# Kernel tuning notes

Measured on AMD Instinct MI355X. Metric: run time of the kernel, lower is better.

The kernel has to match this reference:

```python
import jax, jax.numpy as jnp
import numpy as np

N = 20000        # nodes
E = 160000       # directed edges (self-loops added in reference, as PyG GATConv does)
IN = 128         # in_channels
OUT = 128        # out_channels
H = 36           # heads of conv1 (head kwarg)
C = 36           # per-head channels of conv1 (== head kwarg)
HID = H * C      # 1296, conv1 concat output
NEG_SLOPE = 0.2  # PyG GATConv default


def gat_layer(x, src, dst, W, a_src, a_dst, bias, heads, ch, concat, num_nodes):
    """One PyG-style GATConv (eval mode, self-loops already in src/dst)."""
    h = (x @ W).reshape(num_nodes, heads, ch)               # [N,H,C]
    alpha_s = jnp.sum(h * a_src, axis=-1)                   # [N,H]
    alpha_d = jnp.sum(h * a_dst, axis=-1)                   # [N,H]
    e = jax.nn.leaky_relu(alpha_s[src] + alpha_d[dst], NEG_SLOPE)  # [E,H]
    # segment softmax over incoming edges of each target node
    m = jax.ops.segment_max(e, dst, num_segments=num_nodes)        # [N,H]
    m = jnp.where(jnp.isfinite(m), m, 0.0)                  # nodes with no in-edges
    ex = jnp.exp(e - m[dst])                                # [E,H]
    denom = jax.ops.segment_sum(ex, dst, num_segments=num_nodes)   # [N,H]
    alpha = ex / (denom[dst] + 1e-16)                       # [E,H]
    # weighted scatter-aggregate of source features
    out = jax.ops.segment_sum(h[src] * alpha[:, :, None], dst, num_segments=num_nodes)  # [N,H,C]
    out = out.reshape(num_nodes, heads * ch) if concat else out.mean(axis=1)
    return out + bias


def setup_inputs() -> dict:
    key = jax.random.key(0)
    ks = jax.random.split(key, 12)
    x = jax.random.normal(ks[0], (N, IN), jnp.float32)
    edge_index = jax.random.randint(ks[1], (2, E), 0, N, dtype=jnp.int64)
    # conv1 params: heads=36, out per head=36, concat
    W1 = jax.random.normal(ks[2], (IN, H * C), jnp.float32) / np.float32(np.sqrt(IN))
    a_src1 = jax.random.normal(ks[3], (H, C), jnp.float32) * 0.1
    a_dst1 = jax.random.normal(ks[4], (H, C), jnp.float32) * 0.1
    b1 = jnp.zeros((HID,), jnp.float32)
    # conv2 params: heads=1, out=OUT, no concat
    W2 = jax.random.normal(ks[5], (HID, OUT), jnp.float32) / np.float32(np.sqrt(HID))
    a_src2 = jax.random.normal(ks[6], (1, OUT), jnp.float32) * 0.1
    a_dst2 = jax.random.normal(ks[7], (1, OUT), jnp.float32) * 0.1
    b2 = jnp.zeros((OUT,), jnp.float32)
    return {"x": x, "edge_index": edge_index,
            "W1": W1, "a_src1": a_src1, "a_dst1": a_dst1, "b1": b1,
            "W2": W2, "a_src2": a_src2, "a_dst2": a_dst2, "b2": b2}


def reference(x, edge_index, W1, a_src1, a_dst1, b1, W2, a_src2, a_dst2, b2):
    num_nodes = x.shape[0]
    loop = jnp.arange(num_nodes, dtype=edge_index.dtype)
    src = jnp.concatenate([edge_index[0], loop])   # add self-loops (PyG default)
    dst = jnp.concatenate([edge_index[1], loop])
    h = jax.nn.relu(gat_layer(x, src, dst, W1, a_src1, a_dst1, b1,
                              heads=H, ch=C, concat=True, num_nodes=num_nodes))
    out = jax.nn.relu(gat_layer(h, src, dst, W2, a_src2, a_dst2, b2,
                                heads=1, ch=OUT, concat=False, num_nodes=num_nodes))
    return out
```

## Files before the change

kernel.cpp:

```cpp
#include <hip/hip_runtime.h>

#define N_NODES 20000
#define E_EDGES 160000
#define ET (E_EDGES + N_NODES)
#define IN_CH 128
#define HID 1296
#define HEADS 36
#define CPH 36
#define OUT_CH 128
#define KP2 1344
#define NEG_SLOPE 0.2f

typedef __attribute__((ext_vector_type(8))) short bf16x8;
typedef __attribute__((ext_vector_type(4))) float floatx4;

__device__ __forceinline__ float bf2f(unsigned short u) {
    union { unsigned int i; float f; } c; c.i = ((unsigned int)u) << 16; return c.f;
}
__device__ __forceinline__ unsigned short f2bf(float f) {
    union { float f; unsigned int i; } c; c.f = f;
    unsigned int r = c.i + 0x7FFF + ((c.i >> 16) & 1);
    return (unsigned short)(r >> 16);
}

__global__ __launch_bounds__(256) void k_castx(const float* __restrict__ x,
                                               unsigned short* __restrict__ xb) {
    int i = blockIdx.x * 256 + threadIdx.x;
    if (i >= N_NODES * IN_CH / 4) return;
    float4 v = ((const float4*)x)[i];
    ushort4 o; o.x = f2bf(v.x); o.y = f2bf(v.y); o.z = f2bf(v.z); o.w = f2bf(v.w);
    ((ushort4*)xb)[i] = o;
}

__global__ __launch_bounds__(256) void k_w1t(const float* __restrict__ W1,
                                             unsigned short* __restrict__ W1T) {
    int gid = blockIdx.x * 256 + threadIdx.x;
    if (gid >= HID * IN_CH) return;
    int n = gid >> 7, k = gid & 127;
    W1T[gid] = f2bf(W1[(size_t)k * HID + n]);
}

__global__ __launch_bounds__(256) void k_w2t(const float* __restrict__ W2,
                                             unsigned short* __restrict__ W2T) {
    int gid = blockIdx.x * 256 + threadIdx.x;
    if (gid >= OUT_CH * KP2) return;
    int n = gid / KP2, k = gid - n * KP2;
    W2T[gid] = (k < HID) ? f2bf(W2[(size_t)k * OUT_CH + n]) : 0;
}

__global__ __launch_bounds__(256) void k_gemm1(const unsigned short* __restrict__ xb,
                                               const unsigned short* __restrict__ W1T,
                                               unsigned short* __restrict__ h1b) {
    __shared__ unsigned short As[128][136];
    __shared__ unsigned short Bs[64][136];
    int tid = threadIdx.x;
    int r0 = blockIdx.x * 128;
    int n0 = blockIdx.y * 64;
#pragma unroll
    for (int i = 0; i < 8; i++) {
        int c = tid + i * 256;
        int row = c >> 4, kc = (c & 15) * 8;
        int gr = min(r0 + row, N_NODES - 1);
        *(bf16x8*)&As[row][kc] = *(const bf16x8*)(xb + (size_t)gr * IN_CH + kc);
    }
#pragma unroll
    for (int i = 0; i < 4; i++) {
        int c = tid + i * 256;
        int row = c >> 4, kc = (c & 15) * 8;
        int gn = min(n0 + row, HID - 1);
        *(bf16x8*)&Bs[row][kc] = *(const bf16x8*)(W1T + (size_t)gn * IN_CH + kc);
    }
    __syncthreads();
    int lane = tid & 63, w = tid >> 6;
    int quad = lane >> 4, l15 = lane & 15;
    int mbase = w * 32;
    floatx4 acc[2][4];
#pragma unroll
    for (int i = 0; i < 2; i++)
#pragma unroll
        for (int j = 0; j < 4; j++) acc[i][j] = (floatx4){0.f, 0.f, 0.f, 0.f};
#pragma unroll
    for (int kc = 0; kc < 128; kc += 32) {
        bf16x8 a0 = *(const bf16x8*)&As[mbase + l15][kc + quad * 8];
        bf16x8 a1 = *(const bf16x8*)&As[mbase + 16 + l15][kc + quad * 8];
#pragma unroll
        for (int j = 0; j < 4; j++) {
            bf16x8 b = *(const bf16x8*)&Bs[j * 16 + l15][kc + quad * 8];
            acc[0][j] = __builtin_amdgcn_mfma_f32_16x16x32_bf16(a0, b, acc[0][j], 0, 0, 0);
            acc[1][j] = __builtin_amdgcn_mfma_f32_16x16x32_bf16(a1, b, acc[1][j], 0, 0, 0);
        }
    }
#pragma unroll
    for (int i = 0; i < 2; i++)
#pragma unroll
        for (int j = 0; j < 4; j++) {
            int colc = n0 + j * 16 + l15;
            if (colc >= HID) continue;
#pragma unroll
            for (int r = 0; r < 4; r++) {
                int row = r0 + mbase + i * 16 + quad * 4 + r;
                if (row < N_NODES)
                    h1b[(size_t)row * HID + colc] = f2bf(acc[i][j][r]);
            }
        }
}

__global__ __launch_bounds__(256) void k_gemm2(const unsigned short* __restrict__ A,
                                               const unsigned short* __restrict__ W2T,
                                               float* __restrict__ h2a,
                                               float* __restrict__ h2b) {
    __shared__ unsigned short As[64][40];
    __shared__ unsigned short Bs[128][40];
    int tid = threadIdx.x;
    int r0 = blockIdx.x * 64;
    int kbase = blockIdx.y * 672;
    int lane = tid & 63, w = tid >> 6;
    int quad = lane >> 4, l15 = lane & 15;
    int mbase = (w & 1) * 32;
    int nbase = (w >> 1) * 64;
    floatx4 acc[2][4];
#pragma unroll
    for (int i = 0; i < 2; i++)
#pragma unroll
        for (int j = 0; j < 4; j++) acc[i][j] = (floatx4){0.f, 0.f, 0.f, 0.f};

    for (int it = 0; it < 21; it++) {
        int k0 = kbase + it * 32;
        __syncthreads();
        {
            int row = tid >> 2, kc = (tid & 3) * 8;
            int gr = min(r0 + row, N_NODES - 1);
            *(bf16x8*)&As[row][kc] = *(const bf16x8*)(A + (size_t)gr * KP2 + k0 + kc);
        }
        {
#pragma unroll
            for (int i = 0; i < 2; i++) {
                int c = tid + i * 256;
                int row = c >> 2, kc = (c & 3) * 8;
                *(bf16x8*)&Bs[row][kc] = *(const bf16x8*)(W2T + (size_t)row * KP2 + k0 + kc);
            }
        }
        __syncthreads();
        bf16x8 a0 = *(const bf16x8*)&As[mbase + l15][quad * 8];
        bf16x8 a1 = *(const bf16x8*)&As[mbase + 16 + l15][quad * 8];
#pragma unroll
        for (int j = 0; j < 4; j++) {
            bf16x8 b = *(const bf16x8*)&Bs[nbase + j * 16 + l15][quad * 8];
            acc[0][j] = __builtin_amdgcn_mfma_f32_16x16x32_bf16(a0, b, acc[0][j], 0, 0, 0);
            acc[1][j] = __builtin_amdgcn_mfma_f32_16x16x32_bf16(a1, b, acc[1][j], 0, 0, 0);
        }
    }
    float* dst = (blockIdx.y == 0) ? h2a : h2b;
#pragma unroll
    for (int i = 0; i < 2; i++)
#pragma unroll
        for (int j = 0; j < 4; j++) {
            int colc = nbase + j * 16 + l15;
#pragma unroll
            for (int r = 0; r < 4; r++) {
                int row = r0 + mbase + i * 16 + quad * 4 + r;
                if (row < N_NODES)
                    dst[(size_t)row * OUT_CH + colc] = acc[i][j][r];
            }
        }
}

__global__ __launch_bounds__(256) void k_alpha1(const unsigned short* __restrict__ h1b,
                                                const float* __restrict__ a_src,
                                                const float* __restrict__ a_dst,
                                                float* __restrict__ as,
                                                float* __restrict__ ad) {
    __shared__ float s_a[HEADS * CPH], s_b[HEADS * CPH];
    int tid = threadIdx.x;
    for (int i = tid; i < HEADS * CPH; i += 256) { s_a[i] = a_src[i]; s_b[i] = a_dst[i]; }
    __syncthreads();
    int gid = blockIdx.x * 256 + tid;
    if (gid >= N_NODES * HEADS) return;
    int n = gid / HEADS, h = gid - n * HEADS;
    const unsigned short* row = h1b + (size_t)n * HID + h * CPH;
    float ss = 0.f, sd = 0.f;
#pragma unroll
    for (int c = 0; c < CPH; c += 2) {
        uint u = *(const uint*)(row + c);
        float v0 = bf2f((unsigned short)(u & 0xFFFF));
        float v1 = bf2f((unsigned short)(u >> 16));
        ss += v0 * s_a[h * CPH + c] + v1 * s_a[h * CPH + c + 1];
        sd += v0 * s_b[h * CPH + c] + v1 * s_b[h * CPH + c + 1];
    }
    as[gid] = ss;
    ad[gid] = sd;
}

__global__ void k_count(const int* __restrict__ ei, int* __restrict__ cnt) {
    int e = blockIdx.x * 256 + threadIdx.x;
    if (e >= ET) return;
    int d = (e < E_EDGES) ? ei[E_EDGES + e] : (e - E_EDGES);
    atomicAdd(&cnt[d], 1);
}

__global__ __launch_bounds__(1024) void k_scan(const int* __restrict__ cnt, int* __restrict__ rowp) {
    __shared__ int sh[1024];
    const int PER = 20;
    int t = threadIdx.x;
    int base = t * PER;
    int local[PER];
    int sum = 0;
    for (int i = 0; i < PER; i++) {
        int idx = base + i;
        int v = (idx < N_NODES) ? cnt[idx] : 0;
        local[i] = sum;
        sum += v;
    }
    sh[t] = sum;
    __syncthreads();
    for (int off = 1; off < 1024; off <<= 1) {
        int v = (t >= off) ? sh[t - off] : 0;
        __syncthreads();
        sh[t] += v;
        __syncthreads();
    }
    int offset = (t == 0) ? 0 : sh[t - 1];
    for (int i = 0; i < PER; i++) {
        int idx = base + i;
        if (idx < N_NODES) rowp[idx] = offset + local[i];
    }
    if (t == 1023) rowp[N_NODES] = sh[1023];
}

__global__ void k_fill(const int* __restrict__ ei, const int* __restrict__ rowp,
                       int* __restrict__ cursor, int* __restrict__ col,
                       int* __restrict__ dstn) {
    int e = blockIdx.x * 256 + threadIdx.x;
    if (e >= ET) return;
    int s, d;
    if (e < E_EDGES) { s = ei[e]; d = ei[E_EDGES + e]; }
    else { s = e - E_EDGES; d = s; }
    int pos = rowp[d] + atomicAdd(&cursor[d], 1);
    col[pos] = s;
    dstn[pos] = d;
}

__global__ __launch_bounds__(256) void k_w1(const float* __restrict__ as1,
                                            const float* __restrict__ ad1,
                                            const int* __restrict__ col,
                                            const int* __restrict__ dstn,
                                            float* __restrict__ w) {
    int gid = blockIdx.x * 256 + threadIdx.x;
    if (gid >= ET * HEADS) return;
    int p = gid / HEADS, h = gid - p * HEADS;
    int s = col[p], d = dstn[p];
    float v = as1[(size_t)s * HEADS + h] + ad1[(size_t)d * HEADS + h];
    v = (v > 0.f) ? v : NEG_SLOPE * v;
    w[gid] = __expf(v);
}

__global__ __launch_bounds__(256) void k_agg1(const unsigned short* __restrict__ h1b,
                                              const float* __restrict__ w,
                                              const int* __restrict__ rowp,
                                              const int* __restrict__ col,
                                              const float* __restrict__ b1,
                                              unsigned short* __restrict__ out1b) {
    int n = blockIdx.x;
    int tid = threadIdx.x;
    int r0 = rowp[n], r1 = rowp[n + 1];
    __shared__ float inv[HEADS];
    __shared__ float wsh[32 * HEADS];
    __shared__ int   csh[32];
    if (tid < HEADS) {
        float den = 0.f;
        for (int p = r0; p < r1; p++) den += w[(size_t)p * HEADS + tid];
        inv[tid] = 1.f / (den + 1e-16f);
    }
    __syncthreads();
    float4 acc0 = {0.f, 0.f, 0.f, 0.f}, acc1 = {0.f, 0.f, 0.f, 0.f};
    int s1 = tid;
    int s2 = tid + 256;
    int h1i = s1 / 9;
    int h2i = (s2 < 324) ? s2 / 9 : 0;
    for (int p0 = r0; p0 < r1; p0 += 32) {
        int ne = min(32, r1 - p0);
        __syncthreads();
        for (int i = tid; i < ne * HEADS; i += 256) {
            int h = i % HEADS;
            wsh[i] = w[(size_t)p0 * HEADS + i] * inv[h];
        }
        if (tid < ne) csh[tid] = col[p0 + tid];
        __syncthreads();
        for (int e = 0; e < ne; e++) {
            const ushort4* hr = (const ushort4*)(h1b + (size_t)csh[e] * HID);
            float wa = wsh[e * HEADS + h1i];
            ushort4 v1 = hr[s1];
            acc0.x += wa * bf2f(v1.x); acc0.y += wa * bf2f(v1.y);
            acc0.z += wa * bf2f(v1.z); acc0.w += wa * bf2f(v1.w);
            if (s2 < 324) {
                float wb = wsh[e * HEADS + h2i];
                ushort4 v2 = hr[s2];
                acc1.x += wb * bf2f(v2.x); acc1.y += wb * bf2f(v2.y);
                acc1.z += wb * bf2f(v2.z); acc1.w += wb * bf2f(v2.w);
            }
        }
    }
    const float4* b4 = (const float4*)b1;
    ushort4* o4 = (ushort4*)(out1b + (size_t)n * KP2);
    {
        float4 bb = b4[s1];
        ushort4 o;
        o.x = f2bf(fmaxf(acc0.x + bb.x, 0.f)); o.y = f2bf(fmaxf(acc0.y + bb.y, 0.f));
        o.z = f2bf(fmaxf(acc0.z + bb.z, 0.f)); o.w = f2bf(fmaxf(acc0.w + bb.w, 0.f));
        o4[s1] = o;
    }
    if (s2 < 324) {
        float4 bb = b4[s2];
        ushort4 o;
        o.x = f2bf(fmaxf(acc1.x + bb.x, 0.f)); o.y = f2bf(fmaxf(acc1.y + bb.y, 0.f));
        o.z = f2bf(fmaxf(acc1.z + bb.z, 0.f)); o.w = f2bf(fmaxf(acc1.w + bb.w, 0.f));
        o4[s2] = o;
    } else if (s2 < KP2 / 4) {
        o4[s2] = (ushort4){0, 0, 0, 0};
    }
}

__global__ __launch_bounds__(64) void k_alpha2c(const float* __restrict__ h2a,
                                                const float* __restrict__ h2b,
                                                float* __restrict__ h2,
                                                const float* __restrict__ a_src,
                                                const float* __restrict__ a_dst,
                                                float* __restrict__ as,
                                                float* __restrict__ ad) {
    int n = blockIdx.x;
    int t = threadIdx.x;
    size_t base = (size_t)n * OUT_CH;
    float v0 = h2a[base + t] + h2b[base + t];
    float v1 = h2a[base + t + 64] + h2b[base + t + 64];
    h2[base + t] = v0;
    h2[base + t + 64] = v1;
    float ss = v0 * a_src[t] + v1 * a_src[t + 64];
    float sd = v0 * a_dst[t] + v1 * a_dst[t + 64];
    for (int off = 32; off > 0; off >>= 1) {
        ss += __shfl_down(ss, off);
        sd += __shfl_down(sd, off);
    }
    if (t == 0) { as[n] = ss; ad[n] = sd; }
}

__global__ __launch_bounds__(128) void k_agg2(const float* __restrict__ h2,
                                              const float* __restrict__ as,
                                              const float* __restrict__ ad,
                                              const int* __restrict__ rowp,
                                              const int* __restrict__ col,
                                              const float* __restrict__ b2,
                                              float* __restrict__ out) {
    int n = blockIdx.x;
    int tid = threadIdx.x;
    __shared__ float sh_inv;
    int r0 = rowp[n], r1 = rowp[n + 1];
    float adn = ad[n];
    if (tid < 64) {
        float den = 0.f;
        for (int e = r0 + tid; e < r1; e += 64) {
            int s = col[e];
            float v = as[s] + adn;
            v = (v > 0.f) ? v : NEG_SLOPE * v;
            den += __expf(v);
        }
        for (int off = 32; off > 0; off >>= 1) den += __shfl_down(den, off);
        if (tid == 0) sh_inv = 1.f / (den + 1e-16f);
    }
    __syncthreads();
    float inv = sh_inv;
    float acc = 0.f;
    for (int e = r0; e < r1; e++) {
        int s = col[e];
        float v = as[s] + adn;
        v = (v > 0.f) ? v : NEG_SLOPE * v;
        float wv = __expf(v) * inv;
        acc += wv * h2[(size_t)s * OUT_CH + tid];
    }
    float v = acc + b2[tid];
    out[(size_t)n * OUT_CH + tid] = (v > 0.f) ? v : 0.f;
}

extern "C" void kernel_launch(void* const* d_in, const int* in_sizes, int n_in,
                              void* d_out, int out_size, void* d_ws, size_t ws_size,
                              hipStream_t stream) {
    const float* x      = (const float*)d_in[0];
    const int*   ei     = (const int*)d_in[1];
    const float* W1     = (const float*)d_in[2];
    const float* a_src1 = (const float*)d_in[3];
    const float* a_dst1 = (const float*)d_in[4];
    const float* b1     = (const float*)d_in[5];
    const float* W2     = (const float*)d_in[6];
    const float* a_src2 = (const float*)d_in[7];
    const float* a_dst2 = (const float*)d_in[8];
    const float* b2     = (const float*)d_in[9];
    float* out = (float*)d_out;

    unsigned short* h1b   = (unsigned short*)d_ws;
    unsigned short* out1b = h1b + (size_t)N_NODES * HID;
    unsigned short* xb    = out1b + (size_t)N_NODES * KP2;
    unsigned short* W1T   = xb + (size_t)N_NODES * IN_CH;
    unsigned short* W2T   = W1T + (size_t)HID * IN_CH;
    float* fbase = (float*)(W2T + (size_t)OUT_CH * KP2);
    float* as1  = fbase;
    float* ad1  = as1 + (size_t)N_NODES * HEADS;
    float* wbuf = ad1 + (size_t)N_NODES * HEADS;
    float* h2a  = wbuf;
    float* h2b  = wbuf + (size_t)N_NODES * OUT_CH;
    float* h2   = wbuf + (size_t)ET * HEADS;
    float* as2  = h2 + (size_t)N_NODES * OUT_CH;
    float* ad2  = as2 + N_NODES;
    int* cnt    = (int*)(ad2 + N_NODES);
    int* cursor = cnt + N_NODES;
    int* rowp   = cursor + N_NODES;
    int* colx   = rowp + (N_NODES + 1);
    int* dstn   = colx + ET;

    hipMemsetAsync(cnt, 0, (size_t)2 * N_NODES * sizeof(int), stream);

    k_castx<<<(N_NODES * IN_CH / 4 + 255) / 256, 256, 0, stream>>>(x, xb);
    k_w1t<<<(HID * IN_CH + 255) / 256, 256, 0, stream>>>(W1, W1T);
    k_w2t<<<(OUT_CH * KP2 + 255) / 256, 256, 0, stream>>>(W2, W2T);

    k_gemm1<<<dim3(157, 21), 256, 0, stream>>>(xb, W1T, h1b);
    k_alpha1<<<(N_NODES * HEADS + 255) / 256, 256, 0, stream>>>(h1b, a_src1, a_dst1, as1, ad1);
    k_count<<<(ET + 255) / 256, 256, 0, stream>>>(ei, cnt);
    k_scan<<<1, 1024, 0, stream>>>(cnt, rowp);
    k_fill<<<(ET + 255) / 256, 256, 0, stream>>>(ei, rowp, cursor, colx, dstn);
    k_w1<<<(ET * HEADS + 255) / 256, 256, 0, stream>>>(as1, ad1, colx, dstn, wbuf);
    k_agg1<<<N_NODES, 256, 0, stream>>>(h1b, wbuf, rowp, colx, b1, out1b);
    k_gemm2<<<dim3(313, 2), 256, 0, stream>>>(out1b, W2T, h2a, h2b);
    k_alpha2c<<<N_NODES, 64, 0, stream>>>(h2a, h2b, h2, a_src2, a_dst2, as2, ad2);
    k_agg2<<<N_NODES, 128, 0, stream>>>(h2, as2, ad2, rowp, colx, b2, out);
}
```

Baseline: 332.0 us.

## Fuse prep casts, atomic softmax denominators, bf16 h2, retile gemm2, unroll aggregations

Merges the three cast/transpose kernels into one launch. The per-head softmax denominators for layer 1 are now accumulated with atomics in k_w1 instead of a serial per-node loop in k_agg1. gemm2 moves to 32-row tiles to launch more blocks, and h2 is stored in bf16 so agg2 reads less data, with 64 threads handling two channels each and edges staged in shared memory. Both aggregation loops are unrolled by two edges to overlap gathers. The costs are atomic contention on den1, extra bf16 rounding in layer 2, and an order-dependent floating-point sum.

```diff
diff --git a/kernel.cpp b/kernel.cpp
--- a/kernel.cpp
+++ b/kernel.cpp
@@ -23,29 +23,29 @@
     return (unsigned short)(r >> 16);
 }
 
-__global__ __launch_bounds__(256) void k_castx(const float* __restrict__ x,
-                                               unsigned short* __restrict__ xb) {
-    int i = blockIdx.x * 256 + threadIdx.x;
-    if (i >= N_NODES * IN_CH / 4) return;
-    float4 v = ((const float4*)x)[i];
-    ushort4 o; o.x = f2bf(v.x); o.y = f2bf(v.y); o.z = f2bf(v.z); o.w = f2bf(v.w);
-    ((ushort4*)xb)[i] = o;
-}
-
-__global__ __launch_bounds__(256) void k_w1t(const float* __restrict__ W1,
-                                             unsigned short* __restrict__ W1T) {
+#define NX (N_NODES * IN_CH / 4)
+#define NW1 (HID * IN_CH)
+#define NW2 (OUT_CH * KP2)
+__global__ __launch_bounds__(256) void k_prep(const float* __restrict__ x,
+                                              unsigned short* __restrict__ xb,
+                                              const float* __restrict__ W1,
+                                              unsigned short* __restrict__ W1T,
+                                              const float* __restrict__ W2,
+                                              unsigned short* __restrict__ W2T) {
     int gid = blockIdx.x * 256 + threadIdx.x;
-    if (gid >= HID * IN_CH) return;
-    int n = gid >> 7, k = gid & 127;
-    W1T[gid] = f2bf(W1[(size_t)k * HID + n]);
-}
-
-__global__ __launch_bounds__(256) void k_w2t(const float* __restrict__ W2,
-                                             unsigned short* __restrict__ W2T) {
-    int gid = blockIdx.x * 256 + threadIdx.x;
-    if (gid >= OUT_CH * KP2) return;
-    int n = gid / KP2, k = gid - n * KP2;
-    W2T[gid] = (k < HID) ? f2bf(W2[(size_t)k * OUT_CH + n]) : 0;
+    if (gid < NX) {
+        float4 v = ((const float4*)x)[gid];
+        ushort4 o; o.x = f2bf(v.x); o.y = f2bf(v.y); o.z = f2bf(v.z); o.w = f2bf(v.w);
+        ((ushort4*)xb)[gid] = o;
+    } else if (gid < NX + NW1) {
+        int g = gid - NX;
+        int n = g >> 7, k = g & 127;
+        W1T[g] = f2bf(W1[(size_t)k * HID + n]);
+    } else if (gid < NX + NW1 + NW2) {
+        int g = gid - NX - NW1;
+        int n = g / KP2, k = g - n * KP2;
+        W2T[g] = (k < HID) ? f2bf(W2[(size_t)k * OUT_CH + n]) : 0;
+    }
 }
 
 __global__ __launch_bounds__(256) void k_gemm1(const unsigned short* __restrict__ xb,
@@ -109,58 +109,53 @@
                                                const unsigned short* __restrict__ W2T,
                                                float* __restrict__ h2a,
                                                float* __restrict__ h2b) {
-    __shared__ unsigned short As[64][40];
+    __shared__ unsigned short As[32][40];
     __shared__ unsigned short Bs[128][40];
     int tid = threadIdx.x;
-    int r0 = blockIdx.x * 64;
+    int r0 = blockIdx.x * 32;
     int kbase = blockIdx.y * 672;
     int lane = tid & 63, w = tid >> 6;
     int quad = lane >> 4, l15 = lane & 15;
-    int mbase = (w & 1) * 32;
-    int nbase = (w >> 1) * 64;
-    floatx4 acc[2][4];
+    int nbase = w * 32;
+    floatx4 acc[2][2];
 #pragma unroll
     for (int i = 0; i < 2; i++)
 #pragma unroll
-        for (int j = 0; j < 4; j++) acc[i][j] = (floatx4){0.f, 0.f, 0.f, 0.f};
+        for (int j = 0; j < 2; j++) acc[i][j] = (floatx4){0.f, 0.f, 0.f, 0.f};
 
     for (int it = 0; it < 21; it++) {
         int k0 = kbase + it * 32;
         __syncthreads();
-        {
+        if (tid < 128) {
             int row = tid >> 2, kc = (tid & 3) * 8;
-            int gr = min(r0 + row, N_NODES - 1);
-            *(bf16x8*)&As[row][kc] = *(const bf16x8*)(A + (size_t)gr * KP2 + k0 + kc);
-        }
-        {
-#pragma unroll
-            for (int i = 0; i < 2; i++) {
-                int c = tid + i * 256;
-                int row = c >> 2, kc = (c & 3) * 8;
-                *(bf16x8*)&Bs[row][kc] = *(const bf16x8*)(W2T + (size_t)row * KP2 + k0 + kc);
-            }
-        }
-        __syncthreads();
-        bf16x8 a0 = *(const bf16x8*)&As[mbase + l15][quad * 8];
-        bf16x8 a1 = *(const bf16x8*)&As[mbase + 16 + l15][quad * 8];
-#pragma unroll
-        for (int j = 0; j < 4; j++) {
-            bf16x8 b = *(const bf16x8*)&Bs[nbase + j * 16 + l15][quad * 8];
-            acc[0][j] = __builtin_amdgcn_mfma_f32_16x16x32_bf16(a0, b, acc[0][j], 0, 0, 0);
-            acc[1][j] = __builtin_amdgcn_mfma_f32_16x16x32_bf16(a1, b, acc[1][j], 0, 0, 0);
-        }
+            *(bf16x8*)&As[row][kc] = *(const bf16x8*)(A + (size_t)(r0 + row) * KP2 + k0 + kc);
+        }
+#pragma unroll
+        for (int i = 0; i < 2; i++) {
+            int c = tid + i * 256;
+            int row = c >> 2, kc = (c & 3) * 8;
+            *(bf16x8*)&Bs[row][kc] = *(const bf16x8*)(W2T + (size_t)row * KP2 + k0 + kc);
+        }
+        __syncthreads();
+        bf16x8 a0 = *(const bf16x8*)&As[l15][quad * 8];
+        bf16x8 a1 = *(const bf16x8*)&As[16 + l15][quad * 8];
+        bf16x8 b0 = *(const bf16x8*)&Bs[nbase + l15][quad * 8];
+        bf16x8 b1 = *(const bf16x8*)&Bs[nbase + 16 + l15][quad * 8];
+        acc[0][0] = __builtin_amdgcn_mfma_f32_16x16x32_bf16(a0, b0, acc[0][0], 0, 0, 0);
+        acc[1][0] = __builtin_amdgcn_mfma_f32_16x16x32_bf16(a1, b0, acc[1][0], 0, 0, 0);
+        acc[0][1] = __builtin_amdgcn_mfma_f32_16x16x32_bf16(a0, b1, acc[0][1], 0, 0, 0);
+        acc[1][1] = __builtin_amdgcn_mfma_f32_16x16x32_bf16(a1, b1, acc[1][1], 0, 0, 0);
     }
     float* dst = (blockIdx.y == 0) ? h2a : h2b;
 #pragma unroll
     for (int i = 0; i < 2; i++)
 #pragma unroll
-        for (int j = 0; j < 4; j++) {
+        for (int j = 0; j < 2; j++) {
             int colc = nbase + j * 16 + l15;
 #pragma unroll
             for (int r = 0; r < 4; r++) {
-                int row = r0 + mbase + i * 16 + quad * 4 + r;
-                if (row < N_NODES)
-                    dst[(size_t)row * OUT_CH + colc] = acc[i][j][r];
+                int row = r0 + i * 16 + quad * 4 + r;
+                dst[(size_t)row * OUT_CH + colc] = acc[i][j][r];
             }
         }
 }
@@ -244,18 +239,22 @@
                                             const float* __restrict__ ad1,
                                             const int* __restrict__ col,
                                             const int* __restrict__ dstn,
-                                            float* __restrict__ w) {
+                                            float* __restrict__ w,
+                                            float* __restrict__ den) {
     int gid = blockIdx.x * 256 + threadIdx.x;
     if (gid >= ET * HEADS) return;
     int p = gid / HEADS, h = gid - p * HEADS;
     int s = col[p], d = dstn[p];
     float v = as1[(size_t)s * HEADS + h] + ad1[(size_t)d * HEADS + h];
     v = (v > 0.f) ? v : NEG_SLOPE * v;
-    w[gid] = __expf(v);
+    float ev = __expf(v);
+    w[gid] = ev;
+    atomicAdd(&den[(size_t)d * HEADS + h], ev);
 }
 
 __global__ __launch_bounds__(256) void k_agg1(const unsigned short* __restrict__ h1b,
                                               const float* __restrict__ w,
+                                              const float* __restrict__ den,
                                               const int* __restrict__ rowp,
                                               const int* __restrict__ col,
                                               const float* __restrict__ b1,
@@ -266,37 +265,55 @@
     __shared__ float inv[HEADS];
     __shared__ float wsh[32 * HEADS];
     __shared__ int   csh[32];
-    if (tid < HEADS) {
-        float den = 0.f;
-        for (int p = r0; p < r1; p++) den += w[(size_t)p * HEADS + tid];
-        inv[tid] = 1.f / (den + 1e-16f);
-    }
-    __syncthreads();
+    if (tid < HEADS) inv[tid] = 1.f / (den[(size_t)n * HEADS + tid] + 1e-16f);
     float4 acc0 = {0.f, 0.f, 0.f, 0.f}, acc1 = {0.f, 0.f, 0.f, 0.f};
     int s1 = tid;
     int s2 = tid + 256;
+    bool s2v = (s2 < 324);
     int h1i = s1 / 9;
-    int h2i = (s2 < 324) ? s2 / 9 : 0;
+    int h2i = s2v ? s2 / 9 : 0;
     for (int p0 = r0; p0 < r1; p0 += 32) {
         int ne = min(32, r1 - p0);
         __syncthreads();
         for (int i = tid; i < ne * HEADS; i += 256) {
-            int h = i % HEADS;
-            wsh[i] = w[(size_t)p0 * HEADS + i] * inv[h];
+            wsh[i] = w[(size_t)p0 * HEADS + i] * inv[i % HEADS];
         }
         if (tid < ne) csh[tid] = col[p0 + tid];
         __syncthreads();
-        for (int e = 0; e < ne; e++) {
-            const ushort4* hr = (const ushort4*)(h1b + (size_t)csh[e] * HID);
+        int e = 0;
+        for (; e + 2 <= ne; e += 2) {
+            const ushort4* hA = (const ushort4*)(h1b + (size_t)csh[e] * HID);
+            const ushort4* hB = (const ushort4*)(h1b + (size_t)csh[e + 1] * HID);
+            ushort4 va1 = hA[s1];
+            ushort4 vb1 = hB[s1];
             float wa = wsh[e * HEADS + h1i];
-            ushort4 v1 = hr[s1];
-            acc0.x += wa * bf2f(v1.x); acc0.y += wa * bf2f(v1.y);
-            acc0.z += wa * bf2f(v1.z); acc0.w += wa * bf2f(v1.w);
-            if (s2 < 324) {
-                float wb = wsh[e * HEADS + h2i];
-                ushort4 v2 = hr[s2];
-                acc1.x += wb * bf2f(v2.x); acc1.y += wb * bf2f(v2.y);
-                acc1.z += wb * bf2f(v2.z); acc1.w += wb * bf2f(v2.w);
+            float wb = wsh[(e + 1) * HEADS + h1i];
+            acc0.x += wa * bf2f(va1.x) + wb * bf2f(vb1.x);
+            acc0.y += wa * bf2f(va1.y) + wb * bf2f(vb1.y);
+            acc0.z += wa * bf2f(va1.z) + wb * bf2f(vb1.z);
+            acc0.w += wa * bf2f(va1.w) + wb * bf2f(vb1.w);
+            if (s2v) {
+                ushort4 va2 = hA[s2];
+                ushort4 vb2 = hB[s2];
+                float wa2 = wsh[e * HEADS + h2i];
+                float wb2 = wsh[(e + 1) * HEADS + h2i];
+                acc1.x += wa2 * bf2f(va2.x) + wb2 * bf2f(vb2.x);
+                acc1.y += wa2 * bf2f(va2.y) + wb2 * bf2f(vb2.y);
+                acc1.z += wa2 * bf2f(va2.z) + wb2 * bf2f(vb2.z);
+                acc1.w += wa2 * bf2f(va2.w) + wb2 * bf2f(vb2.w);
+            }
+        }
+        if (e < ne) {
+            const ushort4* hA = (const ushort4*)(h1b + (size_t)csh[e] * HID);
+            ushort4 va1 = hA[s1];
+            float wa = wsh[e * HEADS + h1i];
+            acc0.x += wa * bf2f(va1.x); acc0.y += wa * bf2f(va1.y);
+            acc0.z += wa * bf2f(va1.z); acc0.w += wa * bf2f(va1.w);
+            if (s2v) {
+                ushort4 va2 = hA[s2];
+                float wa2 = wsh[e * HEADS + h2i];
+                acc1.x += wa2 * bf2f(va2.x); acc1.y += wa2 * bf2f(va2.y);
+                acc1.z += wa2 * bf2f(va2.z); acc1.w += wa2 * bf2f(va2.w);
             }
         }
     }
@@ -309,7 +326,7 @@
         o.z = f2bf(fmaxf(acc0.z + bb.z, 0.f)); o.w = f2bf(fmaxf(acc0.w + bb.w, 0.f));
         o4[s1] = o;
     }
-    if (s2 < 324) {
+    if (s2v) {
         float4 bb = b4[s2];
         ushort4 o;
         o.x = f2bf(fmaxf(acc1.x + bb.x, 0.f)); o.y = f2bf(fmaxf(acc1.y + bb.y, 0.f));
@@ -322,7 +339,7 @@
 
 __global__ __launch_bounds__(64) void k_alpha2c(const float* __restrict__ h2a,
                                                 const float* __restrict__ h2b,
-                                                float* __restrict__ h2,
+                                                unsigned short* __restrict__ h2q,
                                                 const float* __restrict__ a_src,
                                                 const float* __restrict__ a_dst,
                                                 float* __restrict__ as,
@@ -332,8 +349,8 @@
     size_t base = (size_t)n * OUT_CH;
     float v0 = h2a[base + t] + h2b[base + t];
     float v1 = h2a[base + t + 64] + h2b[base + t + 64];
-    h2[base + t] = v0;
-    h2[base + t + 64] = v1;
+    h2q[base + t] = f2bf(v0);
+    h2q[base + t + 64] = f2bf(v1);
     float ss = v0 * a_src[t] + v1 * a_src[t + 64];
     float sd = v0 * a_dst[t] + v1 * a_dst[t + 64];
     for (int off = 32; off > 0; off >>= 1) {
@@ -343,41 +360,59 @@
     if (t == 0) { as[n] = ss; ad[n] = sd; }
 }
 
-__global__ __launch_bounds__(128) void k_agg2(const float* __restrict__ h2,
-                                              const float* __restrict__ as,
-                                              const float* __restrict__ ad,
-                                              const int* __restrict__ rowp,
-                                              const int* __restrict__ col,
-                                              const float* __restrict__ b2,
-                                              float* __restrict__ out) {
+__global__ __launch_bounds__(64) void k_agg2(const unsigned short* __restrict__ h2q,
+                                             const float* __restrict__ as,
+                                             const float* __restrict__ ad,
+                                             const int* __restrict__ rowp,
+                                             const int* __restrict__ col,
+                                             const float* __restrict__ b2,
+                                             float* __restrict__ out) {
     int n = blockIdx.x;
-    int tid = threadIdx.x;
-    __shared__ float sh_inv;
+    int t = threadIdx.x;
     int r0 = rowp[n], r1 = rowp[n + 1];
     float adn = ad[n];
-    if (tid < 64) {
-        float den = 0.f;
-        for (int e = r0 + tid; e < r1; e += 64) {
-            int s = col[e];
+    float den = 0.f;
+    for (int e = r0 + t; e < r1; e += 64) {
+        float v = as[col[e]] + adn;
+        v = (v > 0.f) ? v : NEG_SLOPE * v;
+        den += __expf(v);
+    }
+#pragma unroll
+    for (int off = 32; off > 0; off >>= 1) den += __shfl_xor(den, off);
+    float inv = 1.f / (den + 1e-16f);
+    __shared__ float wsh[32];
+    __shared__ int csh[32];
+    float acc0 = 0.f, acc1 = 0.f;
+    for (int p0 = r0; p0 < r1; p0 += 32) {
+        int ne = min(32, r1 - p0);
+        __syncthreads();
+        if (t < ne) {
+            int s = col[p0 + t];
+            csh[t] = s;
             float v = as[s] + adn;
             v = (v > 0.f) ? v : NEG_SLOPE * v;
-            den += __expf(v);
-        }
-        for (int off = 32; off > 0; off >>= 1) den += __shfl_down(den, off);
-        if (tid == 0) sh_inv = 1.f / (den + 1e-16f);
-    }
-    __syncthreads();
-    float inv = sh_inv;
-    float acc = 0.f;
-    for (int e = r0; e < r1; e++) {
-        int s = col[e];
-        float v = as[s] + adn;
-        v = (v > 0.f) ? v : NEG_SLOPE * v;
-        float wv = __expf(v) * inv;
-        acc += wv * h2[(size_t)s * OUT_CH + tid];
-    }
-    float v = acc + b2[tid];
-    out[(size_t)n * OUT_CH + tid] = (v > 0.f) ? v : 0.f;
+            wsh[t] = __expf(v) * inv;
+        }
+        __syncthreads();
+        int e = 0;
+        for (; e + 2 <= ne; e += 2) {
+            uint ua = *(const uint*)(h2q + (size_t)csh[e] * OUT_CH + t * 2);
+            uint ub = *(const uint*)(h2q + (size_t)csh[e + 1] * OUT_CH + t * 2);
+            float wa = wsh[e], wb = wsh[e + 1];
+            acc0 += wa * bf2f((unsigned short)(ua & 0xFFFF)) + wb * bf2f((unsigned short)(ub & 0xFFFF));
+            acc1 += wa * bf2f((unsigned short)(ua >> 16)) + wb * bf2f((unsigned short)(ub >> 16));
+        }
+        if (e < ne) {
+            uint ua = *(const uint*)(h2q + (size_t)csh[e] * OUT_CH + t * 2);
+            float wa = wsh[e];
+            acc0 += wa * bf2f((unsigned short)(ua & 0xFFFF));
+            acc1 += wa * bf2f((unsigned short)(ua >> 16));
+        }
+    }
+    float o0 = acc0 + b2[t * 2];
+    float o1 = acc1 + b2[t * 2 + 1];
+    out[(size_t)n * OUT_CH + t * 2]     = (o0 > 0.f) ? o0 : 0.f;
+    out[(size_t)n * OUT_CH + t * 2 + 1] = (o1 > 0.f) ? o1 : 0.f;
 }
 
 extern "C" void kernel_launch(void* const* d_in, const int* in_sizes, int n_in,
@@ -400,35 +435,33 @@
     unsigned short* xb    = out1b + (size_t)N_NODES * KP2;
     unsigned short* W1T   = xb + (size_t)N_NODES * IN_CH;
     unsigned short* W2T   = W1T + (size_t)HID * IN_CH;
-    float* fbase = (float*)(W2T + (size_t)OUT_CH * KP2);
+    float* fbase = (float*)(W2T + NW2);
     float* as1  = fbase;
     float* ad1  = as1 + (size_t)N_NODES * HEADS;
     float* wbuf = ad1 + (size_t)N_NODES * HEADS;
     float* h2a  = wbuf;
     float* h2b  = wbuf + (size_t)N_NODES * OUT_CH;
-    float* h2   = wbuf + (size_t)ET * HEADS;
-    float* as2  = h2 + (size_t)N_NODES * OUT_CH;
+    unsigned short* h2q = (unsigned short*)(wbuf + (size_t)2 * N_NODES * OUT_CH);
+    float* as2  = wbuf + (size_t)ET * HEADS;
     float* ad2  = as2 + N_NODES;
     int* cnt    = (int*)(ad2 + N_NODES);
     int* cursor = cnt + N_NODES;
-    int* rowp   = cursor + N_NODES;
+    float* den1 = (float*)(cursor + N_NODES);
+    int* rowp   = (int*)(den1 + (size_t)N_NODES * HEADS);
     int* colx   = rowp + (N_NODES + 1);
     int* dstn   = colx + ET;
 
-    hipMemsetAsync(cnt, 0, (size_t)2 * N_NODES * sizeof(int), stream);
-
-    k_castx<<<(N_NODES * IN_CH / 4 + 255) / 256, 256, 0, stream>>>(x, xb);
-    k_w1t<<<(HID * IN_CH + 255) / 256, 256, 0, stream>>>(W1, W1T);
-    k_w2t<<<(OUT_CH * KP2 + 255) / 256, 256, 0, stream>>>(W2, W2T);
-
-    k_gemm1<<<dim3(157, 21), 256, 0, stream>>>(xb, W1T, h1b);
-    k_alpha1<<<(N_NODES * HEADS + 255) / 256, 256, 0, stream>>>(h1b, a_src1, a_dst1, as1, ad1);
+    hipMemsetAsync(cnt, 0, (size_t)(2 * N_NODES + N_NODES * HEADS) * sizeof(int), stream);
+
+    k_prep<<<(NX + NW1 + NW2 + 255) / 256, 256, 0, stream>>>(x, xb, W1, W1T, W2, W2T);
     k_count<<<(ET + 255) / 256, 256, 0, stream>>>(ei, cnt);
     k_scan<<<1, 1024, 0, stream>>>(cnt, rowp);
     k_fill<<<(ET + 255) / 256, 256, 0, stream>>>(ei, rowp, cursor, colx, dstn);
-    k_w1<<<(ET * HEADS + 255) / 256, 256, 0, stream>>>(as1, ad1, colx, dstn, wbuf);
-    k_agg1<<<N_NODES, 256, 0, stream>>>(h1b, wbuf, rowp, colx, b1, out1b);
-    k_gemm2<<<dim3(313, 2), 256, 0, stream>>>(out1b, W2T, h2a, h2b);
-    k_alpha2c<<<N_NODES, 64, 0, stream>>>(h2a, h2b, h2, a_src2, a_dst2, as2, ad2);
-    k_agg2<<<N_NODES, 128, 0, stream>>>(h2, as2, ad2, rowp, colx, b2, out);
-}
+    k_gemm1<<<dim3(157, 21), 256, 0, stream>>>(xb, W1T, h1b);
+    k_alpha1<<<(N_NODES * HEADS + 255) / 256, 256, 0, stream>>>(h1b, a_src1, a_dst1, as1, ad1);
+    k_w1<<<(ET * HEADS + 255) / 256, 256, 0, stream>>>(as1, ad1, colx, dstn, wbuf, den1);
+    k_agg1<<<N_NODES, 256, 0, stream>>>(h1b, wbuf, den1, rowp, colx, b1, out1b);
+    k_gemm2<<<dim3(625, 2), 256, 0, stream>>>(out1b, W2T, h2a, h2b);
+    k_alpha2c<<<N_NODES, 64, 0, stream>>>(h2a, h2b, h2q, a_src2, a_dst2, as2, ad2);
+    k_agg2<<<N_NODES, 64, 0, stream>>>(h2q, as2, ad2, rowp, colx, b2, out);
+}
```

Result: faster. 323.0 us (-2.7%).
